# Performance work log

Hardware: AMD Instinct MI355X
Metric: run time of the kernel (lower is better)

## Reference

```python
import jax, jax.numpy as jnp
import numpy as np

DIM = 768
HEADS = 12
HEAD_DIM = DIM // HEADS
HIDDEN = int(DIM * 4.0)
EPS = 1e-5
SCALE = HEAD_DIM ** -0.5


def _layernorm(x, g, b):
    m = jnp.mean(x, axis=-1, keepdims=True)
    v = jnp.mean(jnp.square(x - m), axis=-1, keepdims=True)
    return (x - m) * jax.lax.rsqrt(v + EPS) * g + b


def setup_inputs() -> dict:
    key = jax.random.key(0)
    ks = jax.random.split(key, 12)
    B, N = 2, 2048
    s = 0.02
    return {
        "x": jax.random.normal(ks[0], (B, N, DIM), dtype=jnp.float32),
        "mask": jax.random.randint(ks[1], (B, N), 0, 2, dtype=jnp.int32),
        "ln1_g": jnp.ones((DIM,), jnp.float32),
        "ln1_b": jnp.zeros((DIM,), jnp.float32),
        "qkv_w": jax.random.normal(ks[2], (3 * DIM, DIM), jnp.float32) * s,
        "proj_w": jax.random.normal(ks[3], (DIM, DIM), jnp.float32) * s,
        "proj_b": jnp.zeros((DIM,), jnp.float32),
        "ln2_g": jnp.ones((DIM,), jnp.float32),
        "ln2_b": jnp.zeros((DIM,), jnp.float32),
        "fc1_w": jax.random.normal(ks[4], (HIDDEN, DIM), jnp.float32) * s,
        "fc1_b": jnp.zeros((HIDDEN,), jnp.float32),
        "fc2_w": jax.random.normal(ks[5], (DIM, HIDDEN), jnp.float32) * s,
        "fc2_b": jnp.zeros((DIM,), jnp.float32),
    }


def reference(x, mask, ln1_g, ln1_b, qkv_w, proj_w, proj_b, ln2_g, ln2_b,
              fc1_w, fc1_b, fc2_w, fc2_b):
    B, N, C = x.shape
    # --- attention on norm1(x) ---
    h = _layernorm(x, ln1_g, ln1_b)
    qkv = (h @ qkv_w.T).reshape(B, N, 3, HEADS, HEAD_DIM)
    q, k, v = qkv[:, :, 0], qkv[:, :, 1], qkv[:, :, 2]  # [B,N,H,D]
    scores = jnp.einsum('bnhd,bmhd->bhnm', q, k) * SCALE  # [B,H,N,N]
    neg_inf = jnp.finfo(scores.dtype).min
    scores = jnp.where(mask[:, None, None, :] == 1, neg_inf, scores)
    attn = jax.nn.softmax(scores, axis=-1)
    y = jnp.einsum('bhnm,bmhd->bnhd', attn, v).reshape(B, N, C)
    y = y @ proj_w.T + proj_b
    x = x + y
    # --- MLP on norm2(x) ---
    h2 = _layernorm(x, ln2_g, ln2_b)
    h2 = jax.nn.gelu(h2 @ fc1_w.T + fc1_b, approximate=False)
    x = x + (h2 @ fc2_w.T + fc2_b)
    return x
```

## Files before the change

kernel.cpp:

```cpp
#include <hip/hip_runtime.h>
#include <math.h>
#include <float.h>

#define DIM 768
#define HEADS 12
#define HD 64
#define HIDDEN 3072
#define SEQ 2048
#define BATCH 2
#define NTOK (BATCH * SEQ)
#define QKVC (3 * DIM)
#define LN_EPS 1e-5f
#define SC2 0.1803368801111f

typedef unsigned short u16;
typedef __attribute__((ext_vector_type(8))) __bf16 bf16x8;
typedef __attribute__((ext_vector_type(8))) unsigned short u16x8;
typedef __attribute__((ext_vector_type(4))) float f32x4;

__device__ __forceinline__ u16 f2bf(float f) {
    unsigned int u = __builtin_bit_cast(unsigned int, f);
    u += 0x7fffu + ((u >> 16) & 1u);
    return (u16)(u >> 16);
}

__device__ __forceinline__ f32x4 mfma16(u16x8 a, u16x8 b, f32x4 c) {
    return __builtin_amdgcn_mfma_f32_16x16x32_bf16(
        __builtin_bit_cast(bf16x8, a), __builtin_bit_cast(bf16x8, b), c, 0, 0, 0);
}

__device__ __forceinline__ void gl2lds16(const void* g, void* l) {
    __builtin_amdgcn_global_load_lds(
        (const __attribute__((address_space(1))) void*)g,
        (__attribute__((address_space(3))) void*)l, 16, 0, 0);
}

__device__ __forceinline__ float gelu_f(float v) {
    return 0.5f * v * (1.0f + erff(v * 0.70710678118654752f));
}

__global__ __launch_bounds__(256) void cvt_all(const float* __restrict__ qkvw,
                                               const float* __restrict__ projw,
                                               const float* __restrict__ fc1w,
                                               const float* __restrict__ fc2w,
                                               u16* __restrict__ o_qkv,
                                               u16* __restrict__ o_proj,
                                               u16* __restrict__ o_fc1,
                                               u16* __restrict__ o_fc2,
                                               const int* __restrict__ mask,
                                               int* __restrict__ pos,
                                               int* __restrict__ cnt) {
    if (blockIdx.x >= 6912) {
        int b = blockIdx.x - 6912, t = threadIdx.x;
        const int* m = mask + b * SEQ;
        int v[8], s = 0;
#pragma unroll
        for (int j = 0; j < 8; ++j) { v[j] = (m[t * 8 + j] == 1) ? 0 : 1; s += v[j]; }
        __shared__ int red[256];
        red[t] = s;
        __syncthreads();
        for (int off = 1; off < 256; off <<= 1) {
            int x = (t >= off) ? red[t - off] : 0;
            __syncthreads();
            red[t] += x;
            __syncthreads();
        }
        int base = red[t] - s;
#pragma unroll
        for (int j = 0; j < 8; ++j) {
            pos[b * SEQ + t * 8 + j] = v[j] ? base : -1;
            base += v[j];
        }
        if (t == 255) cnt[b] = red[255];
        return;
    }
    long i = (long)(blockIdx.x * 256 + threadIdx.x) * 4;
    const float* s; u16* d; long off;
    if (i < 1769472)      { s = qkvw;  d = o_qkv;  off = i; }
    else if (i < 2359296) { s = projw; d = o_proj; off = i - 1769472; }
    else if (i < 4718592) { s = fc1w;  d = o_fc1;  off = i - 2359296; }
    else                  { s = fc2w;  d = o_fc2;  off = i - 4718592; }
    float4 v = *(const float4*)(s + off);
    ushort4 o;
    o.x = f2bf(v.x); o.y = f2bf(v.y); o.z = f2bf(v.z); o.w = f2bf(v.w);
    *(ushort4*)(d + off) = o;
}

__global__ __launch_bounds__(256) void ln_kernel(const float* __restrict__ x,
                                                 const float* __restrict__ g,
                                                 const float* __restrict__ bta,
                                                 u16* __restrict__ out) {
    int row = blockIdx.x;
    int t = threadIdx.x;
    const float* xr = x + (size_t)row * DIM;
    float v0 = xr[t], v1 = xr[t + 256], v2 = xr[t + 512];
    __shared__ float red[256];
    red[t] = v0 + v1 + v2;
    __syncthreads();
    for (int off = 128; off > 0; off >>= 1) {
        if (t < off) red[t] += red[t + off];
        __syncthreads();
    }
    float mean = red[0] * (1.0f / DIM);
    __syncthreads();
    float d0 = v0 - mean, d1 = v1 - mean, d2 = v2 - mean;
    red[t] = d0 * d0 + d1 * d1 + d2 * d2;
    __syncthreads();
    for (int off = 128; off > 0; off >>= 1) {
        if (t < off) red[t] += red[t + off];
        __syncthreads();
    }
    float rstd = rsqrtf(red[0] * (1.0f / DIM) + LN_EPS);
    u16* orow = out + (size_t)row * DIM;
    orow[t]       = f2bf(d0 * rstd * g[t]       + bta[t]);
    orow[t + 256] = f2bf(d1 * rstd * g[t + 256] + bta[t + 256]);
    orow[t + 512] = f2bf(d2 * rstd * g[t + 512] + bta[t + 512]);
}

__global__ __launch_bounds__(256) void repack_kv(const u16* __restrict__ qkv,
                                                 const int* __restrict__ pos,
                                                 u16* __restrict__ kh,
                                                 u16* __restrict__ vth) {
    int s = blockIdx.x;
    int bh = blockIdx.y;
    int b = bh / HEADS, h = bh % HEADS;
    int t = threadIdx.x;
    __shared__ u16 Vl[64 * 72];
    __shared__ int lpos[64];
    const u16* base = qkv + ((size_t)(b * SEQ + s * 64)) * QKVC + h * HD;
    if (t < 64) lpos[t] = pos[b * SEQ + s * 64 + t];
    {
        int vkey = (t & 31) * 2, vd0 = (t >> 5) * 8;
        const u16* g0 = base + 2 * DIM + (size_t)vkey * QKVC + vd0;
        u16x8 a = *(const u16x8*)g0;
        u16x8 c = *(const u16x8*)(g0 + QKVC);
#pragma unroll
        for (int j = 0; j < 8; ++j) {
            unsigned int pk = (unsigned int)a[j] | ((unsigned int)c[j] << 16);
            *(unsigned int*)(Vl + (vd0 + j) * 72 + vkey) = pk;
        }
    }
    __syncthreads();
    {
        int r = t >> 2, d0 = (t & 3) * 16;
        int p = lpos[r];
        if (p >= 0) {
            const u16* g = base + DIM + (size_t)r * QKVC + d0;
            u16* o = kh + (size_t)bh * (SEQ * HD) + (size_t)p * HD + d0;
            *(uint4*)o = *(const uint4*)g;
            *(uint4*)(o + 8) = *(const uint4*)(g + 8);
        }
    }
    {
        int d = t >> 2, m0 = (t & 3) * 16;
        u16* orow = vth + (size_t)bh * (HD * SEQ) + (size_t)d * SEQ;
#pragma unroll
        for (int j = 0; j < 16; ++j) {
            int p = lpos[m0 + j];
            if (p >= 0) orow[p] = Vl[d * 72 + m0 + j];
        }
    }
}

template <int BM, int BN, int EPI>
__global__ __launch_bounds__(256) void mgemm(const u16* __restrict__ A,
                                             const u16* __restrict__ Bw,
                                             void* __restrict__ Cout,
                                             void* __restrict__ Cout2,
                                             int N, int klen,
                                             const float* __restrict__ bias,
                                             const float* __restrict__ resid) {
    constexpr int WM = BM / 2, WN = BN / 2, NI = WM / 16, NJ = WN / 16;
    constexpr int ACALLS = (BM * 64) / 4096;
    constexpr int BCALLS = (BN * 64) / 4096;
    __shared__ u16 As[BM * 32];
    __shared__ u16 Bs[BN * 32];
    int t = threadIdx.x;
    int w = t >> 6, lane = t & 63;
    int quad = lane >> 4, m16 = lane & 15;
    int K = klen * gridDim.z;
    int kbeg = blockIdx.z * klen, kend = kbeg + klen;
    int row0 = blockIdx.y * BM, col0 = blockIdx.x * BN;
    int lrow = lane >> 2;
    int lkb = (lane & 3) * 16;

    f32x4 acc[NI][NJ] = {};

    for (int k0 = kbeg; k0 < kend; k0 += 32) {
        __syncthreads();
#pragma unroll
        for (int c = 0; c < ACALLS; ++c) {
            int off = (w * ACALLS + c) * 1024;
            int r = (off >> 6) + lrow;
            const u16* g = A + (size_t)(row0 + r) * K + k0 + (lkb >> 1);
            gl2lds16(g, As + (off >> 1));
        }
#pragma unroll
        for (int c = 0; c < BCALLS; ++c) {
            int off = (w * BCALLS + c) * 1024;
            int r = (off >> 6) + lrow;
            const u16* g = Bw + (size_t)(col0 + r) * K + k0 + (lkb >> 1);
            gl2lds16(g, Bs + (off >> 1));
        }
        __syncthreads();
        u16x8 af[NI], bfj[NJ];
#pragma unroll
        for (int i = 0; i < NI; ++i)
            af[i] = *(const u16x8*)(As + ((w >> 1) * WM + 16 * i + m16) * 32 + quad * 8);
#pragma unroll
        for (int j = 0; j < NJ; ++j)
            bfj[j] = *(const u16x8*)(Bs + ((w & 1) * WN + 16 * j + m16) * 32 + quad * 8);
#pragma unroll
        for (int i = 0; i < NI; ++i)
#pragma unroll
            for (int j = 0; j < NJ; ++j)
                acc[i][j] = mfma16(af[i], bfj[j], acc[i][j]);
    }

    void* dst = blockIdx.z ? Cout2 : Cout;
    int wr0 = row0 + (w >> 1) * WM, wc0 = col0 + (w & 1) * WN;
#pragma unroll
    for (int i = 0; i < NI; ++i)
#pragma unroll
        for (int j = 0; j < NJ; ++j) {
            int ccol = wc0 + 16 * j + m16;
#pragma unroll
            for (int r = 0; r < 4; ++r) {
                int crow = wr0 + 16 * i + quad * 4 + r;
                float v = acc[i][j][r];
                if (EPI == 0) {
                    ((u16*)dst)[(size_t)crow * N + ccol] = f2bf(v);
                } else if (EPI == 1) {
                    v += bias[ccol] + resid[(size_t)crow * N + ccol];
                    ((float*)dst)[(size_t)crow * N + ccol] = v;
                } else if (EPI == 2) {
                    v = gelu_f(v + bias[ccol]);
                    ((u16*)dst)[(size_t)crow * N + ccol] = f2bf(v);
                } else {
                    ((float*)dst)[(size_t)crow * N + ccol] = v;
                }
            }
        }
}

__global__ __launch_bounds__(256) void merge_kernel(float* __restrict__ out,
                                                    const float* __restrict__ part,
                                                    const float* __restrict__ bias,
                                                    const float* __restrict__ resid) {
    int i = (blockIdx.x * 256 + threadIdx.x) * 4;
    int col = i % DIM;
    float4 o = *(const float4*)(out + i);
    float4 p = *(const float4*)(part + i);
    float4 rr = *(const float4*)(resid + i);
    float4 bb = *(const float4*)(bias + col);
    o.x += p.x + rr.x + bb.x; o.y += p.y + rr.y + bb.y;
    o.z += p.z + rr.z + bb.z; o.w += p.w + rr.w + bb.w;
    *(float4*)(out + i) = o;
}

__global__ __launch_bounds__(256, 3) void attn_mfma(const u16* __restrict__ qkv,
                                                    const u16* __restrict__ kh,
                                                    const u16* __restrict__ vth,
                                                    const int* __restrict__ cnt,
                                                    u16* __restrict__ y) {
    int gx = gridDim.x;
    int flat = blockIdx.y * gx + blockIdx.x;
    int qt = (flat >> 3) % gx;
    int bh = (flat & 7) + 8 * ((flat >> 3) / gx);
    int b = bh / HEADS, h = bh % HEADS;
    int t = threadIdx.x, w = t >> 6, lane = t & 63;
    int quad = lane >> 4, m16 = lane & 15;
    __shared__ u16 Ks[128 * 64];
    __shared__ u16 Vt[64 * 128];
    __shared__ u16 Pw[4][16 * 136];
    const u16* kbase = kh + (size_t)bh * (SEQ * HD);
    const u16* vbase = vth + (size_t)bh * (SEQ * HD);

    int qrow = b * SEQ + qt * 64 + w * 16 + m16;
    const u16* qp = qkv + (size_t)qrow * QKVC + h * HD + quad * 8;
    u16x8 qf0 = *(const u16x8*)qp;
    u16x8 qf1 = *(const u16x8*)(qp + 32);

    int rloc = lane >> 3, kslot = lane & 7;
    int kchunk = kslot ^ rloc;
    int dloc = lane >> 4, vslot = lane & 15;

    float lsum[4] = {0.f, 0.f, 0.f, 0.f};
    f32x4 O[4] = {};

    int slo = quad ^ (m16 & 7);

    int cntb = cnt[b];
    int ntile = (cntb + 127) >> 7;

    for (int kt = 0; kt < ntile; ++kt) {
        int k0 = kt << 7;
        __syncthreads();
#pragma unroll
        for (int c = 0; c < 4; ++c) {
            int rb = (w * 4 + c) * 8;
            const u16* g = kbase + (size_t)(k0 + rb + rloc) * HD + kchunk * 8;
            gl2lds16(g, Ks + (w * 4 + c) * 512);
        }
#pragma unroll
        for (int c = 0; c < 4; ++c) {
            int d = (w * 4 + c) * 4 + dloc;
            int chunk = vslot ^ (d & 15);
            const u16* g = vbase + (size_t)d * SEQ + k0 + chunk * 8;
            gl2lds16(g, Vt + (w * 4 + c) * 512);
        }
        float kb[8];
#pragma unroll
        for (int nb = 0; nb < 8; ++nb)
            kb[nb] = (k0 + m16 + 16 * nb < cntb) ? 0.0f : -1e30f;
        __syncthreads();

#pragma unroll
        for (int nb = 0; nb < 8; ++nb) {
            const u16* krow = Ks + (m16 + 16 * nb) * 64;
            f32x4 s = {0.f, 0.f, 0.f, 0.f};
            s = mfma16(qf0, *(const u16x8*)(krow + slo * 8), s);
            s = mfma16(qf1, *(const u16x8*)(krow + (slo ^ 4) * 8), s);
#pragma unroll
            for (int r = 0; r < 4; ++r) {
                float p = __builtin_amdgcn_exp2f(s[r] * SC2 + kb[nb]);
                lsum[r] += p;
                Pw[w][(quad * 4 + r) * 136 + m16 + 16 * nb] = f2bf(p);
            }
        }
        u16x8 pf[4];
#pragma unroll
        for (int ks = 0; ks < 4; ++ks)
            pf[ks] = *(const u16x8*)(Pw[w] + m16 * 136 + ks * 32 + quad * 8);
#pragma unroll
        for (int nbd = 0; nbd < 4; ++nbd) {
            const u16* vrow = Vt + (nbd * 16 + m16) * 128;
#pragma unroll
            for (int ks = 0; ks < 4; ++ks) {
                int sl = (quad + 4 * ks) ^ m16;
                O[nbd] = mfma16(pf[ks], *(const u16x8*)(vrow + sl * 8), O[nbd]);
            }
        }
    }
#pragma unroll
    for (int off = 1; off < 16; off <<= 1)
#pragma unroll
        for (int r = 0; r < 4; ++r)
            lsum[r] += __shfl_xor(lsum[r], off);
#pragma unroll
    for (int r = 0; r < 4; ++r) {
        float inv = 1.0f / lsum[r];
        int tok = b * SEQ + qt * 64 + w * 16 + quad * 4 + r;
        u16* yr = y + (size_t)tok * DIM + h * HD + m16;
#pragma unroll
        for (int nbd = 0; nbd < 4; ++nbd) yr[16 * nbd] = f2bf(O[nbd][r] * inv);
    }
}

extern "C" void kernel_launch(void* const* d_in, const int* in_sizes, int n_in,
                              void* d_out, int out_size, void* d_ws, size_t ws_size,
                              hipStream_t stream) {
    const float* x      = (const float*)d_in[0];
    const int*   mask   = (const int*)d_in[1];
    const float* ln1_g  = (const float*)d_in[2];
    const float* ln1_b  = (const float*)d_in[3];
    const float* qkv_w  = (const float*)d_in[4];
    const float* proj_w = (const float*)d_in[5];
    const float* proj_b = (const float*)d_in[6];
    const float* ln2_g  = (const float*)d_in[7];
    const float* ln2_b  = (const float*)d_in[8];
    const float* fc1_w  = (const float*)d_in[9];
    const float* fc1_b  = (const float*)d_in[10];
    const float* fc2_w  = (const float*)d_in[11];
    const float* fc2_b  = (const float*)d_in[12];
    float* out = (float*)d_out;

    char* W = (char*)d_ws;
    u16*   wqkv  = (u16*)(W + 0);
    u16*   wproj = (u16*)(W + 3538944);
    u16*   wfc1  = (u16*)(W + 4718592);
    u16*   wfc2  = (u16*)(W + 9437184);
    u16*   hbuf  = (u16*)(W + 14155776);
    float* x1    = (float*)(W + 20447232);
    int*   posb  = (int*)(W + 20463616);
    int*   cntb  = (int*)(W + 20480000);
    u16*   qkvb  = (u16*)(W + 33030144);
    u16*   ybuf  = (u16*)(W + 51904512);
    u16*   a1    = (u16*)(W + 33030144);
    u16*   khb   = (u16*)(W + 58212352);
    u16*   vthb  = (u16*)(W + 64503808);
    float* pp    = (float*)(W + 58212352);

    cvt_all<<<6914, 256, 0, stream>>>(qkv_w, proj_w, fc1_w, fc2_w,
                                      wqkv, wproj, wfc1, wfc2,
                                      mask, posb, cntb);

    ln_kernel<<<NTOK, 256, 0, stream>>>(x, ln1_g, ln1_b, hbuf);
    mgemm<128, 128, 0><<<dim3(QKVC / 128, NTOK / 128), 256, 0, stream>>>(
        hbuf, wqkv, qkvb, nullptr, QKVC, DIM, nullptr, nullptr);
    repack_kv<<<dim3(SEQ / 64, BATCH * HEADS), 256, 0, stream>>>(qkvb, posb, khb, vthb);
    attn_mfma<<<dim3(SEQ / 64, BATCH * HEADS), 256, 0, stream>>>(
        qkvb, khb, vthb, cntb, ybuf);
    mgemm<128, 64, 1><<<dim3(DIM / 64, NTOK / 128), 256, 0, stream>>>(
        ybuf, wproj, x1, nullptr, DIM, DIM, proj_b, x);
    ln_kernel<<<NTOK, 256, 0, stream>>>(x1, ln2_g, ln2_b, hbuf);
    mgemm<128, 128, 2><<<dim3(HIDDEN / 128, NTOK / 128), 256, 0, stream>>>(
        hbuf, wfc1, a1, nullptr, HIDDEN, DIM, fc1_b, nullptr);
    mgemm<128, 64, 3><<<dim3(DIM / 64, NTOK / 128, 2), 256, 0, stream>>>(
        a1, wfc2, pp, out, DIM, HIDDEN / 2, nullptr, nullptr);
    merge_kernel<<<NTOK * DIM / 1024, 256, 0, stream>>>(out, pp, fc2_b, x1);
}
```

Before: 291.4 us.

## Double GEMM K-step to 64 with XOR-swizzled LDS and fold bias/residual into split-K

The GEMM kernel now stages 64-wide K slices per iteration instead of 32, halving the number of barrier pairs, and stores tiles in LDS with an XOR swizzle on 16-byte chunks to avoid bank conflicts on fragment reads. The fc2 split-K GEMM uses a new epilogue mode that adds bias and residual in the second split, and it remaps block indices to group tiles for L2 locality. The merge kernel becomes a plain add. LDS use per block doubles, which may reduce occupancy.

```diff
diff --git a/kernel.cpp b/kernel.cpp
--- a/kernel.cpp
+++ b/kernel.cpp
@@ -171,53 +171,66 @@
                                              const float* __restrict__ bias,
                                              const float* __restrict__ resid) {
     constexpr int WM = BM / 2, WN = BN / 2, NI = WM / 16, NJ = WN / 16;
-    constexpr int ACALLS = (BM * 64) / 4096;
-    constexpr int BCALLS = (BN * 64) / 4096;
-    __shared__ u16 As[BM * 32];
-    __shared__ u16 Bs[BN * 32];
+    constexpr int ACALLS = (BM * 128) / 4096;
+    constexpr int BCALLS = (BN * 128) / 4096;
+    __shared__ u16 As[BM * 64];
+    __shared__ u16 Bs[BN * 64];
     int t = threadIdx.x;
     int w = t >> 6, lane = t & 63;
     int quad = lane >> 4, m16 = lane & 15;
+    int bx = blockIdx.x, by = blockIdx.y;
+    if (EPI == 4) {
+        int gx = gridDim.x;
+        int flat = by * gx + bx;
+        bx = (flat >> 3) % gx;
+        by = (flat & 7) + 8 * ((flat >> 3) / gx);
+    }
     int K = klen * gridDim.z;
-    int kbeg = blockIdx.z * klen, kend = kbeg + klen;
-    int row0 = blockIdx.y * BM, col0 = blockIdx.x * BN;
-    int lrow = lane >> 2;
-    int lkb = (lane & 3) * 16;
+    int kbeg = blockIdx.z * klen;
+    int row0 = by * BM, col0 = bx * BN;
+    int lrow = lane >> 3;
+    int lk = (lane & 7) ^ lrow;
 
     f32x4 acc[NI][NJ] = {};
 
-    for (int k0 = kbeg; k0 < kend; k0 += 32) {
+    for (int k0 = kbeg; k0 < kbeg + klen; k0 += 64) {
         __syncthreads();
 #pragma unroll
         for (int c = 0; c < ACALLS; ++c) {
-            int off = (w * ACALLS + c) * 1024;
-            int r = (off >> 6) + lrow;
-            const u16* g = A + (size_t)(row0 + r) * K + k0 + (lkb >> 1);
-            gl2lds16(g, As + (off >> 1));
+            int r = (w * ACALLS + c) * 8 + lrow;
+            const u16* g = A + (size_t)(row0 + r) * K + k0 + lk * 8;
+            gl2lds16(g, As + (w * ACALLS + c) * 512);
         }
 #pragma unroll
         for (int c = 0; c < BCALLS; ++c) {
-            int off = (w * BCALLS + c) * 1024;
-            int r = (off >> 6) + lrow;
-            const u16* g = Bw + (size_t)(col0 + r) * K + k0 + (lkb >> 1);
-            gl2lds16(g, Bs + (off >> 1));
-        }
-        __syncthreads();
-        u16x8 af[NI], bfj[NJ];
-#pragma unroll
-        for (int i = 0; i < NI; ++i)
-            af[i] = *(const u16x8*)(As + ((w >> 1) * WM + 16 * i + m16) * 32 + quad * 8);
-#pragma unroll
-        for (int j = 0; j < NJ; ++j)
-            bfj[j] = *(const u16x8*)(Bs + ((w & 1) * WN + 16 * j + m16) * 32 + quad * 8);
-#pragma unroll
-        for (int i = 0; i < NI; ++i)
-#pragma unroll
-            for (int j = 0; j < NJ; ++j)
-                acc[i][j] = mfma16(af[i], bfj[j], acc[i][j]);
-    }
-
-    void* dst = blockIdx.z ? Cout2 : Cout;
+            int r = (w * BCALLS + c) * 8 + lrow;
+            const u16* g = Bw + (size_t)(col0 + r) * K + k0 + lk * 8;
+            gl2lds16(g, Bs + (w * BCALLS + c) * 512);
+        }
+        __syncthreads();
+#pragma unroll
+        for (int ks = 0; ks < 2; ++ks) {
+            u16x8 af[NI], bfj[NJ];
+#pragma unroll
+            for (int i = 0; i < NI; ++i) {
+                int rowL = (w >> 1) * WM + 16 * i + m16;
+                af[i] = *(const u16x8*)(As + rowL * 64 +
+                                        (((ks * 4 + quad) ^ (rowL & 7)) * 8));
+            }
+#pragma unroll
+            for (int j = 0; j < NJ; ++j) {
+                int rowL = (w & 1) * WN + 16 * j + m16;
+                bfj[j] = *(const u16x8*)(Bs + rowL * 64 +
+                                         (((ks * 4 + quad) ^ (rowL & 7)) * 8));
+            }
+#pragma unroll
+            for (int i = 0; i < NI; ++i)
+#pragma unroll
+                for (int j = 0; j < NJ; ++j)
+                    acc[i][j] = mfma16(af[i], bfj[j], acc[i][j]);
+        }
+    }
+
     int wr0 = row0 + (w >> 1) * WM, wc0 = col0 + (w & 1) * WN;
 #pragma unroll
     for (int i = 0; i < NI; ++i)
@@ -229,32 +242,31 @@
                 int crow = wr0 + 16 * i + quad * 4 + r;
                 float v = acc[i][j][r];
                 if (EPI == 0) {
-                    ((u16*)dst)[(size_t)crow * N + ccol] = f2bf(v);
+                    ((u16*)Cout)[(size_t)crow * N + ccol] = f2bf(v);
                 } else if (EPI == 1) {
                     v += bias[ccol] + resid[(size_t)crow * N + ccol];
-                    ((float*)dst)[(size_t)crow * N + ccol] = v;
+                    ((float*)Cout)[(size_t)crow * N + ccol] = v;
                 } else if (EPI == 2) {
                     v = gelu_f(v + bias[ccol]);
-                    ((u16*)dst)[(size_t)crow * N + ccol] = f2bf(v);
+                    ((u16*)Cout)[(size_t)crow * N + ccol] = f2bf(v);
                 } else {
-                    ((float*)dst)[(size_t)crow * N + ccol] = v;
+                    if (blockIdx.z == 0) {
+                        ((float*)Cout)[(size_t)crow * N + ccol] = v;
+                    } else {
+                        v += bias[ccol] + resid[(size_t)crow * N + ccol];
+                        ((float*)Cout2)[(size_t)crow * N + ccol] = v;
+                    }
                 }
             }
         }
 }
 
 __global__ __launch_bounds__(256) void merge_kernel(float* __restrict__ out,
-                                                    const float* __restrict__ part,
-                                                    const float* __restrict__ bias,
-                                                    const float* __restrict__ resid) {
+                                                    const float* __restrict__ part) {
     int i = (blockIdx.x * 256 + threadIdx.x) * 4;
-    int col = i % DIM;
     float4 o = *(const float4*)(out + i);
     float4 p = *(const float4*)(part + i);
-    float4 rr = *(const float4*)(resid + i);
-    float4 bb = *(const float4*)(bias + col);
-    o.x += p.x + rr.x + bb.x; o.y += p.y + rr.y + bb.y;
-    o.z += p.z + rr.z + bb.z; o.w += p.w + rr.w + bb.w;
+    o.x += p.x; o.y += p.y; o.z += p.z; o.w += p.w;
     *(float4*)(out + i) = o;
 }
 
@@ -406,7 +418,7 @@
     ln_kernel<<<NTOK, 256, 0, stream>>>(x1, ln2_g, ln2_b, hbuf);
     mgemm<128, 128, 2><<<dim3(HIDDEN / 128, NTOK / 128), 256, 0, stream>>>(
         hbuf, wfc1, a1, nullptr, HIDDEN, DIM, fc1_b, nullptr);
-    mgemm<128, 64, 3><<<dim3(DIM / 64, NTOK / 128, 2), 256, 0, stream>>>(
-        a1, wfc2, pp, out, DIM, HIDDEN / 2, nullptr, nullptr);
-    merge_kernel<<<NTOK * DIM / 1024, 256, 0, stream>>>(out, pp, fc2_b, x1);
-}
+    mgemm<128, 64, 4><<<dim3(DIM / 64, NTOK / 128, 2), 256, 0, stream>>>(
+        a1, wfc2, pp, out, DIM, HIDDEN / 2, fc2_b, x1);
+    merge_kernel<<<NTOK * DIM / 1024, 256, 0, stream>>>(out, pp);
+}
```

Measured after the change: 264.7 us. 1.1x faster.
